# Kernel tuning notes

Hardware: AMD Instinct MI355X
Metric: run time of the kernel (lower is better)

## Reference

```python
import jax, jax.numpy as jnp
import numpy as np

N_ROWS = 100000   # sparse matrix rows (nodes)
N_COLS = 8192     # input feature dim
UNITS = 128
NNZ = 2000000     # ~20 nonzeros per row


def setup_inputs() -> dict:
    key = jax.random.key(0)
    k1, k2, k3, k4, k5 = jax.random.split(key, 5)
    vals = jax.random.normal(k1, (NNZ,), dtype=jnp.float32)
    rows = jax.random.randint(k2, (NNZ,), 0, N_ROWS, dtype=jnp.int32)
    cols = jax.random.randint(k3, (NNZ,), 0, N_COLS, dtype=jnp.int32)
    # GlorotUniform-style scale for W, matching the TF initializer statistics
    limit = jnp.sqrt(6.0 / (N_COLS + UNITS)).astype(jnp.float32)
    W = jax.random.uniform(k4, (N_COLS, UNITS), dtype=jnp.float32, minval=-limit, maxval=limit)
    b = jax.random.uniform(k5, (UNITS,), dtype=jnp.float32, minval=-limit, maxval=limit)
    return {"vals": vals, "rows": rows, "cols": cols, "W": W, "b": b, "num_rows": N_ROWS}


def reference(vals, rows, cols, W, b, num_rows):
    # sparse (COO) [num_rows, F] @ dense W [F, units]:
    # gather the W row for each nonzero, scale by the nonzero value,
    # then scatter-add into the output row -> segment_sum over `rows`.
    gathered = W[cols] * vals[:, None]            # [nnz, units]
    out = jax.ops.segment_sum(gathered, rows, num_segments=num_rows)  # [num_rows, units]
    return out + b                                 # bias add (use_bias=True)
```

## Files before the change

### kernel.cpp

```cpp
#include <hip/hip_runtime.h>
#include <hip/hip_fp16.h>


#define UNITS 128
#define SCAN_BLK 1024
#define BROW 98
#define CBROW 784
#define NCC 128
#define CH3 4096
#define PER 40
#define OCAP 1024
#define SLOTS 40
#define OVF_CAP 256
#define SENT (1023 << 13)


__global__ __launch_bounds__(512, 8) void partition_kernel(
        const float* __restrict__ vals, const int* __restrict__ rows,
        const int* __restrict__ cols, const float* __restrict__ W,
        __half2* __restrict__ Wh, int* __restrict__ ocur,
        float2* __restrict__ sortedA, float2* __restrict__ ovfseg,
        int nnz, int nbcc, int nch, int wn2) {
    __shared__ float2 sStage[CH3];
    __shared__ unsigned char sBkt[CH3];
    __shared__ int hist[NCC];
    __shared__ int excl[NCC];
    __shared__ int cnt[NCC];

    const int t = threadIdx.x;
    const int lane = t & 63;
    const int w = t >> 6;
    const int bb = blockIdx.x;

    {
        const float2* W2 = (const float2*)W;
        int stride = gridDim.x * 512;
        for (int i = bb * 512 + t; i < wn2; i += stride)
            Wh[i] = __float22half2_rn(W2[i]);
    }

    const int chunk0 = bb * CH3;
    int n = nnz - chunk0;
    if (n > CH3) n = CH3;

    if (t < NCC) hist[t] = 0;
    __syncthreads();

    int rbuf[8];
#pragma unroll
    for (int j = 0; j < 8; ++j) {
        int r = j * 512 + t;
        int rv = -1;
        if (r < n) {
            rv = rows[chunk0 + r];
            atomicAdd(&hist[rv / CBROW], 1);
        }
        rbuf[j] = rv;
    }
    __syncthreads();

    if (w == 0) {
        int a0 = hist[2 * lane], a1 = hist[2 * lane + 1];
        int ps = a0 + a1;
        int inc = ps;
#pragma unroll
        for (int o = 1; o < 64; o <<= 1) {
            int u = __shfl_up(inc, o);
            if (lane >= o) inc += u;
        }
        int e0 = inc - ps;
        cnt[2 * lane] = a0;  cnt[2 * lane + 1] = a1;
        excl[2 * lane] = e0; excl[2 * lane + 1] = e0 + a0;
        hist[2 * lane] = e0; hist[2 * lane + 1] = e0 + a0;
    }
    __syncthreads();

#pragma unroll
    for (int j = 0; j < 8; ++j) {
        int rv = rbuf[j];
        if (rv >= 0) {
            int r = j * 512 + t;
            int bkt = rv / CBROW;
            int rlo = rv - bkt * CBROW;
            int pos = atomicAdd(&hist[bkt], 1);
            float v = vals[chunk0 + r];
            int col = cols[chunk0 + r];
            sStage[pos] = make_float2(v, __int_as_float(col | (rlo << 13)));
            sBkt[pos] = (unsigned char)bkt;
        }
    }
    __syncthreads();

    const size_t rowsz = (size_t)nch * PER;
    for (int s = t; s < n; s += 512) {
        float2 e = sStage[s];
        int bkt = sBkt[s];
        int local = s - excl[bkt];
        if (local < PER) {
            sortedA[(size_t)bkt * rowsz + (size_t)bb * PER + local] = e;
        } else {
            int o = atomicAdd(&ocur[bkt * 16], 1);
            if (o < OCAP) ovfseg[bkt * OCAP + o] = e;
        }
    }
    for (int u = t; u < NCC * PER; u += 512) {
        int bkt = u / PER, sl = u - bkt * PER;
        if (bkt < nbcc) {
            int cb = cnt[bkt]; if (cb > PER) cb = PER;
            if (sl >= cb)
                sortedA[(size_t)bkt * rowsz + (size_t)bb * PER + sl] =
                    make_float2(0.f, __int_as_float(SENT));
        }
    }
}


__global__ __launch_bounds__(512, 8) void fused_sort_compute_kernel(
        const float2* __restrict__ A, const int* __restrict__ ocur,
        const float2* __restrict__ ovfseg, const __half2* __restrict__ Wh,
        const float* __restrict__ b, float* __restrict__ out,
        int nchPER, int NR) {
    __shared__ float2 st[BROW * SLOTS];
    __shared__ float2 ovf[OVF_CAP];
    __shared__ int cnt_s[BROW + 6];
    __shared__ int ovf_n;
    const int t = threadIdx.x;
    const int lane = t & 63;
    const int w = t >> 6;

    const int nwg = gridDim.x;
    const int orig = blockIdx.x;
    const int q = nwg >> 3, r8 = nwg & 7, xcd = orig & 7, idx = orig >> 3;
    const int f = (xcd < r8 ? xcd * (q + 1) : r8 * (q + 1) + (xcd - r8) * q) + idx;

    const int c = f >> 3, sb = f & 7;
    const int r0 = f * BROW;
    const int rlo0 = sb * BROW;
    const size_t base = (size_t)c * nchPER;

    const float2 bias = ((const float2*)b)[lane];

    if (t < BROW + 6) cnt_s[t] = 0;
    if (t == 0) ovf_n = 0;
    for (int i = t; i < BROW * SLOTS; i += 512)
        st[i] = make_float2(0.f, __int_as_float(0));
    __syncthreads();

    const float4* A4 = (const float4*)(A + base);
    const int seg2 = nchPER >> 1;
    for (int k2 = t; k2 < seg2; k2 += 512) {
        float4 qv = A4[k2];
        {
            int pk = __float_as_int(qv.y);
            unsigned rl = (unsigned)(pk >> 13) - rlo0;
            if (rl < BROW) {
                int p = atomicAdd(&cnt_s[rl], 1);
                if (p < SLOTS) st[rl * SLOTS + p] = make_float2(qv.x, __int_as_float(pk & 8191));
                else {
                    int qn = atomicAdd(&ovf_n, 1);
                    if (qn < OVF_CAP) ovf[qn] = make_float2(qv.x, __int_as_float((pk & 8191) | (rl << 13)));
                }
            }
        }
        {
            int pk = __float_as_int(qv.w);
            unsigned rl = (unsigned)(pk >> 13) - rlo0;
            if (rl < BROW) {
                int p = atomicAdd(&cnt_s[rl], 1);
                if (p < SLOTS) st[rl * SLOTS + p] = make_float2(qv.z, __int_as_float(pk & 8191));
                else {
                    int qn = atomicAdd(&ovf_n, 1);
                    if (qn < OVF_CAP) ovf[qn] = make_float2(qv.z, __int_as_float((pk & 8191) | (rl << 13)));
                }
            }
        }
    }
    {
        int on0 = ocur[c * 16];
        if (on0 > OCAP) on0 = OCAP;
        for (int k = t; k < on0; k += 512) {
            float2 e = ovfseg[c * OCAP + k];
            int pk = __float_as_int(e.y);
            unsigned rl = (unsigned)(pk >> 13) - rlo0;
            if (rl < BROW) {
                int p = atomicAdd(&cnt_s[rl], 1);
                if (p < SLOTS) st[rl * SLOTS + p] = make_float2(e.x, __int_as_float(pk & 8191));
                else {
                    int qn = atomicAdd(&ovf_n, 1);
                    if (qn < OVF_CAP) ovf[qn] = make_float2(e.x, __int_as_float((pk & 8191) | (rl << 13)));
                }
            }
        }
    }
    __syncthreads();

    const int on = (ovf_n > OVF_CAP) ? OVF_CAP : ovf_n;
    for (int rA = w; rA < BROW; rA += 16) {
        const int rB = rA + 8;
        const bool hasB = (rB < BROW);
        int cA = cnt_s[rA]; if (cA > SLOTS) cA = SLOTS;
        int cB = 0;
        if (hasB) { cB = cnt_s[rB]; if (cB > SLOTS) cB = SLOTS; }
        const float2* sA = &st[rA * SLOTS];
        const float2* sB = &st[(hasB ? rB : rA) * SLOTS];
        int m = (cA > cB) ? cA : cB;
        m = (m + 3) & ~3;
        float axA0 = 0.f, ayA0 = 0.f, axA1 = 0.f, ayA1 = 0.f;
        float axB0 = 0.f, ayB0 = 0.f, axB1 = 0.f, ayB1 = 0.f;
        for (int k = 0; k < m; k += 4) {
            float2 a0 = sA[k], a1 = sA[k + 1], a2 = sA[k + 2], a3 = sA[k + 3];
            float2 b0 = sB[k], b1 = sB[k + 1], b2 = sB[k + 2], b3 = sB[k + 3];
            int ca0 = __float_as_int(a0.y) & 8191;
            int ca1 = __float_as_int(a1.y) & 8191;
            int ca2 = __float_as_int(a2.y) & 8191;
            int ca3 = __float_as_int(a3.y) & 8191;
            int cb0 = __float_as_int(b0.y) & 8191;
            int cb1 = __float_as_int(b1.y) & 8191;
            int cb2 = __float_as_int(b2.y) & 8191;
            int cb3 = __float_as_int(b3.y) & 8191;
            float2 wa0 = __half22float2(Wh[ca0 * 64 + lane]);
            float2 wa1 = __half22float2(Wh[ca1 * 64 + lane]);
            float2 wa2 = __half22float2(Wh[ca2 * 64 + lane]);
            float2 wa3 = __half22float2(Wh[ca3 * 64 + lane]);
            float2 wb0 = __half22float2(Wh[cb0 * 64 + lane]);
            float2 wb1 = __half22float2(Wh[cb1 * 64 + lane]);
            float2 wb2 = __half22float2(Wh[cb2 * 64 + lane]);
            float2 wb3 = __half22float2(Wh[cb3 * 64 + lane]);
            axA0 += a0.x * wa0.x; ayA0 += a0.x * wa0.y;
            axA1 += a1.x * wa1.x; ayA1 += a1.x * wa1.y;
            axA0 += a2.x * wa2.x; ayA0 += a2.x * wa2.y;
            axA1 += a3.x * wa3.x; ayA1 += a3.x * wa3.y;
            axB0 += b0.x * wb0.x; ayB0 += b0.x * wb0.y;
            axB1 += b1.x * wb1.x; ayB1 += b1.x * wb1.y;
            axB0 += b2.x * wb2.x; ayB0 += b2.x * wb2.y;
            axB1 += b3.x * wb3.x; ayB1 += b3.x * wb3.y;
        }
        {
            int grow = r0 + rA;
            if (grow < NR) {
                for (int q2 = 0; q2 < on; ++q2) {
                    float2 eo = ovf[q2];
                    int pk = __float_as_int(eo.y);
                    if ((pk >> 13) == rA) {
                        float2 wv = __half22float2(Wh[(pk & 8191) * 64 + lane]);
                        axA0 += eo.x * wv.x; ayA0 += eo.x * wv.y;
                    }
                }
                ((float2*)out)[(size_t)grow * 64 + lane] =
                    make_float2(axA0 + axA1 + bias.x, ayA0 + ayA1 + bias.y);
            }
        }
        if (hasB) {
            int grow = r0 + rB;
            if (grow < NR) {
                for (int q2 = 0; q2 < on; ++q2) {
                    float2 eo = ovf[q2];
                    int pk = __float_as_int(eo.y);
                    if ((pk >> 13) == rB) {
                        float2 wv = __half22float2(Wh[(pk & 8191) * 64 + lane]);
                        axB0 += eo.x * wv.x; ayB0 += eo.x * wv.y;
                    }
                }
                ((float2*)out)[(size_t)grow * 64 + lane] =
                    make_float2(axB0 + axB1 + bias.x, ayB0 + ayB1 + bias.y);
            }
        }
    }
}


__global__ void hist_kernel(const int* __restrict__ rows, int* __restrict__ counts, int nnz) {
    int i = blockIdx.x * blockDim.x + threadIdx.x;
    if (i < nnz) atomicAdd(&counts[rows[i]], 1);
}

__global__ void scan1_kernel(const int* __restrict__ counts, int* __restrict__ tmp,
                             int* __restrict__ bsums, int NR, int NS) {
    __shared__ int s[SCAN_BLK];
    int t = threadIdx.x;
    int i = blockIdx.x * SCAN_BLK + t;
    int x = (i < NR) ? counts[i] : 0;
    s[t] = x;
    __syncthreads();
    for (int off = 1; off < SCAN_BLK; off <<= 1) {
        int v = (t >= off) ? s[t - off] : 0;
        __syncthreads();
        s[t] += v;
        __syncthreads();
    }
    if (i < NS) tmp[i] = s[t] - x;
    if (t == SCAN_BLK - 1) bsums[blockIdx.x] = s[SCAN_BLK - 1];
}

__global__ void scan2_kernel(int* __restrict__ bsums, int nb) {
    if (threadIdx.x == 0 && blockIdx.x == 0) {
        int run = 0;
        for (int i = 0; i < nb; ++i) { int c = bsums[i]; bsums[i] = run; run += c; }
    }
}

__global__ void scan3_kernel(const int* __restrict__ tmp, const int* __restrict__ bsums,
                             int* __restrict__ row_start, int* __restrict__ cursor,
                             int NR, int NS) {
    int i = blockIdx.x * blockDim.x + threadIdx.x;
    if (i < NS) {
        int v = tmp[i] + bsums[i >> 10];
        row_start[i] = v;
        if (i < NR) cursor[i] = v;
    }
}

__global__ void scatter_sort_kernel(const float* __restrict__ vals, const int* __restrict__ rows,
                                    const int* __restrict__ cols, int* __restrict__ cursor,
                                    float2* __restrict__ sorted, int nnz) {
    int i = blockIdx.x * blockDim.x + threadIdx.x;
    if (i < nnz) {
        int r = rows[i];
        int p = atomicAdd(&cursor[r], 1);
        sorted[p] = make_float2(vals[i], __int_as_float(cols[i]));
    }
}

__global__ void compute_kernel(const float2* __restrict__ sorted, const int* __restrict__ row_start,
                               const float* __restrict__ W, const float* __restrict__ b,
                               float* __restrict__ out, int NR) {
    int lane = threadIdx.x & 63;
    int wv = threadIdx.x >> 6;
    int row = blockIdx.x * 4 + wv;
    if (row >= NR) return;
    int start = row_start[row];
    int end   = row_start[row + 1];
    const float2* W2 = (const float2*)W;
    float accx0 = 0.f, accy0 = 0.f, accx1 = 0.f, accy1 = 0.f;
    for (int base = start; base < end; base += 64) {
        int m = end - base;
        if (m > 64) m = 64;
        float2 p = make_float2(0.f, __int_as_float(0));
        if (lane < m) p = sorted[base + lane];
        int vi = __float_as_int(p.x);
        int ci = __float_as_int(p.y);
        int rounds = (m + 3) & ~3;
        for (int j = 0; j < rounds; j += 4) {
            float v0 = __int_as_float(__builtin_amdgcn_readlane(vi, j));
            int   c0 = __builtin_amdgcn_readlane(ci, j);
            float v1 = __int_as_float(__builtin_amdgcn_readlane(vi, j + 1));
            int   c1 = __builtin_amdgcn_readlane(ci, j + 1);
            float v2 = __int_as_float(__builtin_amdgcn_readlane(vi, j + 2));
            int   c2 = __builtin_amdgcn_readlane(ci, j + 2);
            float v3 = __int_as_float(__builtin_amdgcn_readlane(vi, j + 3));
            int   c3 = __builtin_amdgcn_readlane(ci, j + 3);
            float2 w0 = W2[c0 * 64 + lane];
            float2 w1 = W2[c1 * 64 + lane];
            float2 w2 = W2[c2 * 64 + lane];
            float2 w3 = W2[c3 * 64 + lane];
            accx0 += v0 * w0.x; accy0 += v0 * w0.y;
            accx1 += v1 * w1.x; accy1 += v1 * w1.y;
            accx0 += v2 * w2.x; accy0 += v2 * w2.y;
            accx1 += v3 * w3.x; accy1 += v3 * w3.y;
        }
    }
    float2 bb = ((const float2*)b)[lane];
    ((float2*)out)[(size_t)row * 64 + lane] =
        make_float2(accx0 + accx1 + bb.x, accy0 + accy1 + bb.y);
}


__global__ void init_bias_kernel(float* __restrict__ out, const float* __restrict__ b, int total4) {
    const float4* b4 = (const float4*)b;
    float4* out4 = (float4*)out;
    int stride = gridDim.x * blockDim.x;
    for (int j = blockIdx.x * blockDim.x + threadIdx.x; j < total4; j += stride)
        out4[j] = b4[j & 31];
}

__global__ void scatter_atomic_kernel(const float* __restrict__ vals, const int* __restrict__ rows,
                                      const int* __restrict__ cols, const float* __restrict__ W,
                                      float* __restrict__ out, int nnz) {
    long long idx = (long long)blockIdx.x * blockDim.x + threadIdx.x;
    int i = (int)(idx >> 5);
    int c = (int)(idx & 31);
    if (i >= nnz) return;
    int row = rows[i], col = cols[i];
    float v = vals[i];
    float4 w = ((const float4*)W)[col * 32 + c];
    float* o = out + (size_t)row * UNITS + (c << 2);
    atomicAdd(o + 0, v * w.x);
    atomicAdd(o + 1, v * w.y);
    atomicAdd(o + 2, v * w.z);
    atomicAdd(o + 3, v * w.w);
}

extern "C" void kernel_launch(void* const* d_in, const int* in_sizes, int n_in,
                              void* d_out, int out_size, void* d_ws, size_t ws_size,
                              hipStream_t stream) {
    const float* vals = (const float*)d_in[0];
    const int*   rows = (const int*)d_in[1];
    const int*   cols = (const int*)d_in[2];
    const float* W    = (const float*)d_in[3];
    const float* b    = (const float*)d_in[4];
    float* out = (float*)d_out;

    const int nnz = in_sizes[0];
    const int NW  = in_sizes[3];
    const int NR  = out_size / UNITS;
    const int NS  = NR + 1;
    const int NB  = (NS + SCAN_BLK - 1) / SCAN_BLK;
    const int nbf  = (NR + BROW - 1) / BROW;
    const int nbcc = (NR + CBROW - 1) / CBROW;
    const int nch  = (nnz + CH3 - 1) / CH3;
    const int nchPER = nch * PER;

    auto align = [](size_t x) { return (x + 255) & ~(size_t)255; };

    size_t off_ocur    = 0;
    size_t off_wh      = align(off_ocur + (size_t)NCC * 16 * 4);
    size_t off_sortedA = align(off_wh + (size_t)NW * 2);
    size_t off_ovf     = align(off_sortedA + (size_t)nbcc * (size_t)nchPER * 8);
    size_t needed_full = off_ovf + (size_t)NCC * OCAP * 8;

    size_t t2_counts   = 0;
    size_t t2_tmp      = align(t2_counts + (size_t)NR * 4);
    size_t t2_bsums    = align(t2_tmp    + (size_t)NS * 4);
    size_t t2_rowstart = align(t2_bsums  + (size_t)NB * 4);
    size_t t2_cursor   = align(t2_rowstart + (size_t)NS * 4);
    size_t t2_sorted   = align(t2_cursor + (size_t)NR * 4);
    size_t needed_r2   = t2_sorted + (size_t)nnz * 8;

    char* ws = (char*)d_ws;

    if (ws_size >= needed_full && nbcc >= 1 && nbcc <= NCC && nch >= 1 && NR >= 1) {
        int*     ocur    = (int*)(ws + off_ocur);
        __half2* Wh      = (__half2*)(ws + off_wh);
        float2*  sortedA = (float2*)(ws + off_sortedA);
        float2*  ovfseg  = (float2*)(ws + off_ovf);

        hipMemsetAsync(ocur, 0, (size_t)NCC * 16 * 4, stream);
        partition_kernel<<<nch, 512, 0, stream>>>(vals, rows, cols, W, Wh,
                                                  ocur, sortedA, ovfseg,
                                                  nnz, nbcc, nch, NW / 2);
        fused_sort_compute_kernel<<<nbf, 512, 0, stream>>>(sortedA, ocur, ovfseg,
                                                           Wh, b, out, nchPER, NR);
    } else if (ws_size >= needed_r2) {
        int*    counts    = (int*)(ws + t2_counts);
        int*    tmp       = (int*)(ws + t2_tmp);
        int*    bsums     = (int*)(ws + t2_bsums);
        int*    row_start = (int*)(ws + t2_rowstart);
        int*    cursor    = (int*)(ws + t2_cursor);
        float2* sorted    = (float2*)(ws + t2_sorted);

        hipMemsetAsync(counts, 0, (size_t)NR * 4, stream);
        {
            int block = 256, grid = (nnz + block - 1) / block;
            hist_kernel<<<grid, block, 0, stream>>>(rows, counts, nnz);
        }
        scan1_kernel<<<NB, SCAN_BLK, 0, stream>>>(counts, tmp, bsums, NR, NS);
        scan2_kernel<<<1, 64, 0, stream>>>(bsums, NB);
        {
            int block = 256, grid = (NS + block - 1) / block;
            scan3_kernel<<<grid, block, 0, stream>>>(tmp, bsums, row_start, cursor, NR, NS);
        }
        {
            int block = 256, grid = (nnz + block - 1) / block;
            scatter_sort_kernel<<<grid, block, 0, stream>>>(vals, rows, cols, cursor, sorted, nnz);
        }
        {
            int grid = (NR + 3) / 4;
            compute_kernel<<<grid, 256, 0, stream>>>(sorted, row_start, W, b, out, NR);
        }
    } else {
        int total4 = out_size / 4;
        int block = 256;
        int grid = (total4 + block - 1) / block;
        init_bias_kernel<<<grid, block, 0, stream>>>(out, b, total4);
        long long total_threads = (long long)nnz * 32;
        long long g2 = (total_threads + block - 1) / block;
        scatter_atomic_kernel<<<(int)g2, block, 0, stream>>>(vals, rows, cols, W, out, nnz);
    }
}
```

Before: 150.6 us.

## Sort partition chunks by fine row-block and read only own sub-range

The partition kernel now builds a 1024-bucket histogram at fine row-block granularity (98 rows) and writes, for each chunk, a per-fine-block byte offset table and a fill count into its coarse-bucket cell. Sentinel padding of unused slots is removed. Each compute block reads the offsets and loads only the entries belonging to its own 98-row block, instead of scanning the whole coarse bucket segment shared by 8 blocks. This is meant to cut redundant global reads by about 8x and to drop the sentinel writes. In exchange it adds small offset arrays, a block-wide scan in partition, and narrower scalar loads in a per-thread variable-length loop, which may diverge.

```diff
diff --git a/kernel.cpp b/kernel.cpp
--- a/kernel.cpp
+++ b/kernel.cpp
@@ -7,12 +7,12 @@
 #define BROW 98
 #define CBROW 784
 #define NCC 128
+#define NFB 1024
 #define CH3 4096
 #define PER 40
-#define OCAP 1024
+#define OCAP 512
 #define SLOTS 40
 #define OVF_CAP 256
-#define SENT (1023 << 13)
 
 
 __global__ __launch_bounds__(512, 8) void partition_kernel(
@@ -20,12 +20,13 @@
         const int* __restrict__ cols, const float* __restrict__ W,
         __half2* __restrict__ Wh, int* __restrict__ ocur,
         float2* __restrict__ sortedA, float2* __restrict__ ovfseg,
+        unsigned char* __restrict__ offs, unsigned char* __restrict__ fill,
         int nnz, int nbcc, int nch, int wn2) {
     __shared__ float2 sStage[CH3];
     __shared__ unsigned char sBkt[CH3];
-    __shared__ int hist[NCC];
-    __shared__ int excl[NCC];
-    __shared__ int cnt[NCC];
+    __shared__ int hist[NFB];
+    __shared__ int fexcl[NFB];
+    __shared__ int wsum[8];
 
     const int t = threadIdx.x;
     const int lane = t & 63;
@@ -43,7 +44,7 @@
     int n = nnz - chunk0;
     if (n > CH3) n = CH3;
 
-    if (t < NCC) hist[t] = 0;
+    hist[t] = 0; hist[t + 512] = 0;
     __syncthreads();
 
     int rbuf[8];
@@ -53,14 +54,14 @@
         int rv = -1;
         if (r < n) {
             rv = rows[chunk0 + r];
-            atomicAdd(&hist[rv / CBROW], 1);
+            atomicAdd(&hist[rv / BROW], 1);
         }
         rbuf[j] = rv;
     }
     __syncthreads();
 
-    if (w == 0) {
-        int a0 = hist[2 * lane], a1 = hist[2 * lane + 1];
+    {
+        int a0 = hist[2 * t], a1 = hist[2 * t + 1];
         int ps = a0 + a1;
         int inc = ps;
 #pragma unroll
@@ -68,21 +69,39 @@
             int u = __shfl_up(inc, o);
             if (lane >= o) inc += u;
         }
-        int e0 = inc - ps;
-        cnt[2 * lane] = a0;  cnt[2 * lane + 1] = a1;
-        excl[2 * lane] = e0; excl[2 * lane + 1] = e0 + a0;
-        hist[2 * lane] = e0; hist[2 * lane + 1] = e0 + a0;
-    }
-    __syncthreads();
+        if (lane == 63) wsum[w] = inc;
+        __syncthreads();
+        int wbase = 0;
+        for (int i = 0; i < w; ++i) wbase += wsum[i];
+        int excl = wbase + inc - ps;
+        fexcl[2 * t] = excl;     fexcl[2 * t + 1] = excl + a0;
+        hist[2 * t]  = excl;     hist[2 * t + 1]  = excl + a0;
+    }
+    __syncthreads();
+
+    {
+        int f0 = 2 * t, f1 = 2 * t + 1;
+        int v0 = fexcl[f0] - fexcl[(f0 >> 3) << 3]; if (v0 > PER) v0 = PER;
+        int v1 = fexcl[f1] - fexcl[(f1 >> 3) << 3]; if (v1 > PER) v1 = PER;
+        offs[(size_t)bb * NFB + f0] = (unsigned char)v0;
+        offs[(size_t)bb * NFB + f1] = (unsigned char)v1;
+        if (t < NCC) {
+            int end = (t == NCC - 1) ? n : fexcl[(t + 1) * 8];
+            int bc = end - fexcl[t * 8];
+            if (bc > PER) bc = PER;
+            fill[(size_t)bb * NCC + t] = (unsigned char)bc;
+        }
+    }
 
 #pragma unroll
     for (int j = 0; j < 8; ++j) {
         int rv = rbuf[j];
         if (rv >= 0) {
             int r = j * 512 + t;
-            int bkt = rv / CBROW;
+            int fb = rv / BROW;
+            int bkt = fb >> 3;
             int rlo = rv - bkt * CBROW;
-            int pos = atomicAdd(&hist[bkt], 1);
+            int pos = atomicAdd(&hist[fb], 1);
             float v = vals[chunk0 + r];
             int col = cols[chunk0 + r];
             sStage[pos] = make_float2(v, __int_as_float(col | (rlo << 13)));
@@ -95,7 +114,7 @@
     for (int s = t; s < n; s += 512) {
         float2 e = sStage[s];
         int bkt = sBkt[s];
-        int local = s - excl[bkt];
+        int local = s - fexcl[bkt << 3];
         if (local < PER) {
             sortedA[(size_t)bkt * rowsz + (size_t)bb * PER + local] = e;
         } else {
@@ -103,23 +122,15 @@
             if (o < OCAP) ovfseg[bkt * OCAP + o] = e;
         }
     }
-    for (int u = t; u < NCC * PER; u += 512) {
-        int bkt = u / PER, sl = u - bkt * PER;
-        if (bkt < nbcc) {
-            int cb = cnt[bkt]; if (cb > PER) cb = PER;
-            if (sl >= cb)
-                sortedA[(size_t)bkt * rowsz + (size_t)bb * PER + sl] =
-                    make_float2(0.f, __int_as_float(SENT));
-        }
-    }
 }
 
 
 __global__ __launch_bounds__(512, 8) void fused_sort_compute_kernel(
         const float2* __restrict__ A, const int* __restrict__ ocur,
-        const float2* __restrict__ ovfseg, const __half2* __restrict__ Wh,
+        const float2* __restrict__ ovfseg, const unsigned char* __restrict__ offs,
+        const unsigned char* __restrict__ fill, const __half2* __restrict__ Wh,
         const float* __restrict__ b, float* __restrict__ out,
-        int nchPER, int NR) {
+        int nch, int NR) {
     __shared__ float2 st[BROW * SLOTS];
     __shared__ float2 ovf[OVF_CAP];
     __shared__ int cnt_s[BROW + 6];
@@ -136,7 +147,8 @@
     const int c = f >> 3, sb = f & 7;
     const int r0 = f * BROW;
     const int rlo0 = sb * BROW;
-    const size_t base = (size_t)c * nchPER;
+    const size_t rowsz = (size_t)nch * PER;
+    const float2* bktbase = A + (size_t)c * rowsz;
 
     const float2 bias = ((const float2*)b)[lane];
 
@@ -146,31 +158,21 @@
         st[i] = make_float2(0.f, __int_as_float(0));
     __syncthreads();
 
-    const float4* A4 = (const float4*)(A + base);
-    const int seg2 = nchPER >> 1;
-    for (int k2 = t; k2 < seg2; k2 += 512) {
-        float4 qv = A4[k2];
-        {
-            int pk = __float_as_int(qv.y);
+    for (int k = t; k < nch; k += 512) {
+        int o0 = offs[(size_t)k * NFB + f];
+        int o1 = (sb < 7) ? (int)offs[(size_t)k * NFB + f + 1]
+                          : (int)fill[(size_t)k * NCC + c];
+        const float2* cell = bktbase + (size_t)k * PER;
+        for (int j = o0; j < o1; ++j) {
+            float2 e = cell[j];
+            int pk = __float_as_int(e.y);
             unsigned rl = (unsigned)(pk >> 13) - rlo0;
             if (rl < BROW) {
                 int p = atomicAdd(&cnt_s[rl], 1);
-                if (p < SLOTS) st[rl * SLOTS + p] = make_float2(qv.x, __int_as_float(pk & 8191));
+                if (p < SLOTS) st[rl * SLOTS + p] = make_float2(e.x, __int_as_float(pk & 8191));
                 else {
                     int qn = atomicAdd(&ovf_n, 1);
-                    if (qn < OVF_CAP) ovf[qn] = make_float2(qv.x, __int_as_float((pk & 8191) | (rl << 13)));
-                }
-            }
-        }
-        {
-            int pk = __float_as_int(qv.w);
-            unsigned rl = (unsigned)(pk >> 13) - rlo0;
-            if (rl < BROW) {
-                int p = atomicAdd(&cnt_s[rl], 1);
-                if (p < SLOTS) st[rl * SLOTS + p] = make_float2(qv.z, __int_as_float(pk & 8191));
-                else {
-                    int qn = atomicAdd(&ovf_n, 1);
-                    if (qn < OVF_CAP) ovf[qn] = make_float2(qv.z, __int_as_float((pk & 8191) | (rl << 13)));
+                    if (qn < OVF_CAP) ovf[qn] = make_float2(e.x, __int_as_float((pk & 8191) | (rl << 13)));
                 }
             }
         }
@@ -408,15 +410,16 @@
     const int nbf  = (NR + BROW - 1) / BROW;
     const int nbcc = (NR + CBROW - 1) / CBROW;
     const int nch  = (nnz + CH3 - 1) / CH3;
-    const int nchPER = nch * PER;
 
     auto align = [](size_t x) { return (x + 255) & ~(size_t)255; };
 
     size_t off_ocur    = 0;
     size_t off_wh      = align(off_ocur + (size_t)NCC * 16 * 4);
     size_t off_sortedA = align(off_wh + (size_t)NW * 2);
-    size_t off_ovf     = align(off_sortedA + (size_t)nbcc * (size_t)nchPER * 8);
-    size_t needed_full = off_ovf + (size_t)NCC * OCAP * 8;
+    size_t off_ovf     = align(off_sortedA + (size_t)nbcc * (size_t)nch * PER * 8);
+    size_t off_offs    = align(off_ovf + (size_t)NCC * OCAP * 8);
+    size_t off_fill    = align(off_offs + (size_t)nch * NFB);
+    size_t needed_full = off_fill + (size_t)nch * NCC;
 
     size_t t2_counts   = 0;
     size_t t2_tmp      = align(t2_counts + (size_t)NR * 4);
@@ -428,18 +431,22 @@
 
     char* ws = (char*)d_ws;
 
-    if (ws_size >= needed_full && nbcc >= 1 && nbcc <= NCC && nch >= 1 && NR >= 1) {
-        int*     ocur    = (int*)(ws + off_ocur);
-        __half2* Wh      = (__half2*)(ws + off_wh);
-        float2*  sortedA = (float2*)(ws + off_sortedA);
-        float2*  ovfseg  = (float2*)(ws + off_ovf);
+    if (ws_size >= needed_full && nbcc >= 1 && nbcc <= NCC && nbf <= NFB &&
+        nch >= 1 && NR >= 1) {
+        int*           ocur    = (int*)(ws + off_ocur);
+        __half2*       Wh      = (__half2*)(ws + off_wh);
+        float2*        sortedA = (float2*)(ws + off_sortedA);
+        float2*        ovfseg  = (float2*)(ws + off_ovf);
+        unsigned char* offs    = (unsigned char*)(ws + off_offs);
+        unsigned char* fill    = (unsigned char*)(ws + off_fill);
 
         hipMemsetAsync(ocur, 0, (size_t)NCC * 16 * 4, stream);
         partition_kernel<<<nch, 512, 0, stream>>>(vals, rows, cols, W, Wh,
-                                                  ocur, sortedA, ovfseg,
+                                                  ocur, sortedA, ovfseg, offs, fill,
                                                   nnz, nbcc, nch, NW / 2);
         fused_sort_compute_kernel<<<nbf, 512, 0, stream>>>(sortedA, ocur, ovfseg,
-                                                           Wh, b, out, nchPER, NR);
+                                                           offs, fill, Wh, b, out,
+                                                           nch, NR);
     } else if (ws_size >= needed_r2) {
         int*    counts    = (int*)(ws + t2_counts);
         int*    tmp       = (int*)(ws + t2_tmp);
```

New measurement: 153.2 us. About the same (+1.7%).
